# Kernel tuning notes

Measured on AMD Instinct MI355X. Metric: run time of the kernel, lower is better.

## Reference

```python
import jax, jax.numpy as jnp
import numpy as np

SEQ_LEN = 2048
D_MODEL = 1024
K = 32
B = 16
CP = K * (K + 1) // 2  # 528


def _spectral_filters(seq_len: int, k: int) -> np.ndarray:
    # Hankel matrix Z_ij = 2 / ((i+j)^3 - (i+j)), 1-indexed
    e = np.arange(1, seq_len + 1, dtype=np.float64)
    ipj = e[:, None] + e[None, :]
    Z = 2.0 / (ipj ** 3 - ipj)
    sigma, phi = np.linalg.eigh(Z)
    sk = np.clip(sigma[-k:], 1e-9, None)
    return (phi[:, -k:] * sk ** 0.25).astype(np.float32)


# static upper-triangular index pattern and sqrt(2) off-diagonal scaling
_IU0, _IU1 = np.triu_indices(K)
_SCALE = np.where(_IU0 == _IU1, 1.0, np.sqrt(2.0)).astype(np.float32)


def setup_inputs() -> dict:
    key = jax.random.key(0)
    ks = jax.random.split(key, 8)
    filters = jnp.asarray(_spectral_filters(SEQ_LEN, K))
    x = jax.random.normal(ks[0], (B, SEQ_LEN, D_MODEL), dtype=jnp.float32)
    pre_w = jax.random.normal(ks[1], (SEQ_LEN, D_MODEL), dtype=jnp.float32) / np.sqrt(D_MODEL)
    pre_b = jnp.zeros((SEQ_LEN,), dtype=jnp.float32)
    qp_w = jax.random.normal(ks[2], (CP, K), dtype=jnp.float32) / np.sqrt(K)
    qp_b = jnp.zeros((CP,), dtype=jnp.float32)
    o_w = jax.random.normal(ks[3], (D_MODEL, CP), dtype=jnp.float32) / np.sqrt(CP)
    o_b = jnp.zeros((D_MODEL,), dtype=jnp.float32)
    decay = jnp.ones((SEQ_LEN,), dtype=jnp.float32)
    return {
        'x': x,
        'pre_w': pre_w, 'pre_b': pre_b,
        'q_filters': filters,          # learnable copy
        'k_filters': filters,          # fixed buffer copy
        'qp_w': qp_w, 'qp_b': qp_b,
        'o_w': o_w, 'o_b': o_b,
        'decay': decay,
    }


def reference(x, pre_w, pre_b, q_filters, k_filters, qp_w, qp_b, o_w, o_b, decay):
    # pre_proj: (B,T,d_model) -> (B,T,seq_len)
    x_proj = x @ pre_w.T + pre_b
    # spectral projections onto top-K filters: (B,T,K)
    Q = jnp.einsum('bti,ik->btk', x_proj, q_filters)
    Q = Q @ qp_w.T + qp_b                      # (B,T,CP)
    V = jnp.einsum('bti,ik->btk', x_proj, k_filters)
    # symmetric outer product compressed to upper triangle, off-diag * sqrt(2)
    iu0 = jnp.asarray(_IU0)
    iu1 = jnp.asarray(_IU1)
    scale = jnp.asarray(_SCALE)
    Z = V[..., iu0] * V[..., iu1] * scale      # (B,T,CP), avoids (B,T,K,K)
    Z = Z * decay[None, :, None]
    H = jnp.cumsum(Z, axis=1)                  # causal state accumulation
    Y = Q * H
    return Y @ o_w.T + o_b                     # (B,T,d_model)
```

## Files before the change

### kernel.cpp

```cpp
#include <hip/hip_runtime.h>
#include <hip/hip_bf16.h>
#include <math.h>

#define T_SEQ   2048
#define DM      1024
#define KF      32
#define BATCH   16
#define CPDIM   528
#define KPAD    544
#define YSTR    552
#define QVSTR   36
#define MROWS   (BATCH * T_SEQ)
#define NCHUNK  32
#define TCHUNK  64

typedef __bf16 bf16x8 __attribute__((ext_vector_type(8)));
typedef float f32x4 __attribute__((ext_vector_type(4)));
typedef unsigned uint2v __attribute__((ext_vector_type(2)));

__device__ __forceinline__ unsigned packsplit(float v) {
  unsigned u = __float_as_uint(v);
  unsigned h = (u + 0x7fffu + ((u >> 16) & 1u)) & 0xffff0000u;
  float rr = v - __uint_as_float(h);
  return h | (__float_as_uint(rr) >> 16);
}

__device__ __forceinline__ unsigned short f2bf(float f) {
  unsigned u = __float_as_uint(f);
  return (unsigned short)((u + 0x7fffu + ((u >> 16) & 1u)) >> 16);
}
__device__ __forceinline__ float bf2f(unsigned short h) {
  return __uint_as_float((unsigned)h << 16);
}

__device__ __forceinline__ void gload16(const void* g, void* l) {
  __builtin_amdgcn_global_load_lds(
      (const __attribute__((address_space(1))) unsigned*)g,
      (__attribute__((address_space(3))) unsigned*)l, 16, 0, 0);
}

__global__ __launch_bounds__(256) void k_fold_part(const float* __restrict__ pre_w,
                                                   const float* __restrict__ qf,
                                                   const float* __restrict__ kfil,
                                                   float* __restrict__ Wp) {
  const int sc = blockIdx.x;
  const int it = blockIdx.y;
  const int s0 = sc * 64, i0 = it * 64;
  const int tid = threadIdx.x;
  __shared__ float fs[64][64];
  __shared__ float ps[64][64];
  for (int idx = tid; idx < 4096; idx += 256) {
    const int s = idx >> 6, c = idx & 63;
    fs[s][c] = (c < KF) ? qf[(s0 + s) * KF + c] : kfil[(s0 + s) * KF + c - KF];
    ps[s][c] = pre_w[(size_t)(s0 + s) * DM + i0 + c];
  }
  __syncthreads();
  const int i = tid & 63;
  const int kb = tid >> 6;
  float acc[16] = {};
  for (int s = 0; s < 64; ++s) {
    const float pv = ps[s][i];
    const float4 f0 = *reinterpret_cast<const float4*>(&fs[s][kb * 16 + 0]);
    const float4 f1 = *reinterpret_cast<const float4*>(&fs[s][kb * 16 + 4]);
    const float4 f2 = *reinterpret_cast<const float4*>(&fs[s][kb * 16 + 8]);
    const float4 f3 = *reinterpret_cast<const float4*>(&fs[s][kb * 16 + 12]);
    acc[0]  = fmaf(pv, f0.x, acc[0]);  acc[1]  = fmaf(pv, f0.y, acc[1]);
    acc[2]  = fmaf(pv, f0.z, acc[2]);  acc[3]  = fmaf(pv, f0.w, acc[3]);
    acc[4]  = fmaf(pv, f1.x, acc[4]);  acc[5]  = fmaf(pv, f1.y, acc[5]);
    acc[6]  = fmaf(pv, f1.z, acc[6]);  acc[7]  = fmaf(pv, f1.w, acc[7]);
    acc[8]  = fmaf(pv, f2.x, acc[8]);  acc[9]  = fmaf(pv, f2.y, acc[9]);
    acc[10] = fmaf(pv, f2.z, acc[10]); acc[11] = fmaf(pv, f2.w, acc[11]);
    acc[12] = fmaf(pv, f3.x, acc[12]); acc[13] = fmaf(pv, f3.y, acc[13]);
    acc[14] = fmaf(pv, f3.z, acc[14]); acc[15] = fmaf(pv, f3.w, acc[15]);
  }
#pragma unroll
  for (int j = 0; j < 16; ++j)
    Wp[((size_t)sc * 64 + kb * 16 + j) * DM + i0 + i] = acc[j];
}

__global__ __launch_bounds__(256) void k_foldred_bias(const float* __restrict__ Wp,
                                                      const float* __restrict__ pre_b,
                                                      const float* __restrict__ qf,
                                                      const float* __restrict__ kfil,
                                                      unsigned short* __restrict__ Wt_hi,
                                                      unsigned short* __restrict__ Wt_lo,
                                                      float* __restrict__ bias64) {
  if (blockIdx.x == 256) {
    __shared__ float part[4][64];
    const int k = threadIdx.x & 63;
    const int q = threadIdx.x >> 6;
    float acc = 0.f;
    for (int s = q * 512; s < (q + 1) * 512; ++s) {
      const float fv = (k < KF) ? qf[s * KF + k] : kfil[s * KF + k - KF];
      acc = fmaf(pre_b[s], fv, acc);
    }
    part[q][k] = acc;
    __syncthreads();
    if (threadIdx.x < 64)
      bias64[threadIdx.x] = part[0][k] + part[1][k] + part[2][k] + part[3][k];
    return;
  }
  const int idx = blockIdx.x * 256 + threadIdx.x;
  float acc = 0.f;
#pragma unroll
  for (int sc = 0; sc < NCHUNK; ++sc)
    acc += Wp[(size_t)sc * 64 * DM + idx];
  const unsigned pk = packsplit(acc);
  Wt_hi[idx] = (unsigned short)(pk >> 16);
  Wt_lo[idx] = (unsigned short)(pk & 0xffffu);
}

__global__ __launch_bounds__(256) void k_q0v_cs(const float* __restrict__ x,
                                                const unsigned short* __restrict__ Wt_hi,
                                                const unsigned short* __restrict__ Wt_lo,
                                                const float* __restrict__ bias64,
                                                const float* __restrict__ decay,
                                                float* __restrict__ Q0V,
                                                float* __restrict__ S) {
  __shared__ float Xs[3][64 * 32];
  __shared__ unsigned short Wh[3][64 * 32];
  __shared__ unsigned short Wl[3][64 * 32];
  __shared__ float vs2[64 * 32];
  __shared__ float dec2[64];
  const int tid = threadIdx.x;
  const int m0 = blockIdx.x * 64;
  const int w = tid >> 6, l = tid & 63;
  const int g = l >> 4, r = l & 15;

  f32x4 acc[4] = {};

  auto stage = [&](int buf, int k0) {
#pragma unroll
    for (int q = 0; q < 2; ++q) {
      const int c = q * 256 + tid;
      const int row = c >> 3, sl = c & 7;
      const int col4 = (sl ^ (row & 7)) * 4;
      gload16(&x[(size_t)(m0 + row) * DM + k0 + col4], &Xs[buf][c * 4]);
    }
    {
      const int row = tid >> 2, sl = tid & 3;
      const int colh = (sl ^ ((row >> 1) & 3)) * 8;
      gload16(&Wt_hi[(size_t)row * DM + k0 + colh], &Wh[buf][tid * 8]);
      gload16(&Wt_lo[(size_t)row * DM + k0 + colh], &Wl[buf][tid * 8]);
    }
  };

  auto compute = [&](int cur) {
    const int arow = w * 16 + r;
    const int sx = (2 * g) ^ (arow & 7);
    const int sy = (2 * g + 1) ^ (arow & 7);
    const f32x4 pX = *reinterpret_cast<const f32x4*>(&Xs[cur][arow * 32 + sx * 4]);
    const f32x4 pY = *reinterpret_cast<const f32x4*>(&Xs[cur][arow * 32 + sy * 4]);
    unsigned pk[8];
#pragma unroll
    for (int e = 0; e < 4; ++e) { pk[e] = packsplit(pX[e]); pk[4 + e] = packsplit(pY[e]); }
    union { unsigned u[4]; bf16x8 v; } ah, al;
#pragma unroll
    for (int j = 0; j < 4; ++j) {
      ah.u[j] = (pk[2 * j] >> 16) | (pk[2 * j + 1] & 0xffff0000u);
      al.u[j] = (pk[2 * j] & 0xffffu) | (pk[2 * j + 1] << 16);
    }
    bf16x8 bh[4], bl[4];
#pragma unroll
    for (int n = 0; n < 4; ++n) {
      const int brow = n * 16 + r;
      const int bs = g ^ ((brow >> 1) & 3);
      const int off = brow * 32 + bs * 8;
      bh[n] = *reinterpret_cast<const bf16x8*>(&Wh[cur][off]);
      bl[n] = *reinterpret_cast<const bf16x8*>(&Wl[cur][off]);
    }
#pragma unroll
    for (int n = 0; n < 4; ++n) {
      acc[n] = __builtin_amdgcn_mfma_f32_16x16x32_bf16(bh[n], ah.v, acc[n], 0, 0, 0);
      acc[n] = __builtin_amdgcn_mfma_f32_16x16x32_bf16(bh[n], al.v, acc[n], 0, 0, 0);
      acc[n] = __builtin_amdgcn_mfma_f32_16x16x32_bf16(bl[n], ah.v, acc[n], 0, 0, 0);
    }
  };

  if (tid < 64) dec2[tid] = decay[(m0 & 2047) + tid];

  stage(0, 0);
  stage(1, 32);

  for (int base = 0; base < 30; base += 3) {
#pragma unroll
    for (int sub = 0; sub < 3; ++sub) {
      const int it = base + sub;
      asm volatile("s_waitcnt vmcnt(4)" ::: "memory");
      __builtin_amdgcn_s_barrier();
      __builtin_amdgcn_sched_barrier(0);
      stage((sub + 2) % 3, (it + 2) * 32);
      compute(sub);
    }
  }
  asm volatile("s_waitcnt vmcnt(4)" ::: "memory");
  __builtin_amdgcn_s_barrier();
  __builtin_amdgcn_sched_barrier(0);
  compute(0);
  asm volatile("s_waitcnt vmcnt(0)" ::: "memory");
  __builtin_amdgcn_s_barrier();
  __builtin_amdgcn_sched_barrier(0);
  compute(1);

  const int trow = w * 16 + r;
  const int row_o = m0 + trow;
#pragma unroll
  for (int n = 0; n < 4; ++n) {
    const int col_o = n * 16 + g * 4;
    const float4 bb = *reinterpret_cast<const float4*>(&bias64[col_o]);
    float4 v;
    v.x = acc[n][0] + bb.x; v.y = acc[n][1] + bb.y;
    v.z = acc[n][2] + bb.z; v.w = acc[n][3] + bb.w;
    *reinterpret_cast<float4*>(&Q0V[(size_t)row_o * 64 + col_o]) = v;
    if (n >= 2)
      *reinterpret_cast<float4*>(&vs2[trow * 32 + (n - 2) * 16 + g * 4]) = v;
  }
  __syncthreads();

  const int b = m0 >> 11, ch = (m0 & 2047) >> 6;
#pragma unroll
  for (int pass = 0; pass < 3; ++pass) {
    const int c = tid + pass * 256;
    if (c < CPDIM) {
      int i = 0, rem = c;
      while (rem >= KF - i) { rem -= KF - i; ++i; }
      const int j = i + rem;
      const float sc = (i == j) ? 1.0f : 1.41421356237309515f;
      float h = 0.f;
#pragma unroll 4
      for (int t = 0; t < TCHUNK; ++t)
        h = fmaf(vs2[t * KF + i] * vs2[t * KF + j], dec2[t], h);
      S[(size_t)(b * NCHUNK + ch) * CPDIM + c] = h * sc;
    }
  }
}

__global__ __launch_bounds__(576) void k_scanchunks(float* __restrict__ S) {
  const int b = blockIdx.x;
  const int c = threadIdx.x;
  if (c >= CPDIM) return;
  float v[NCHUNK];
#pragma unroll
  for (int ch = 0; ch < NCHUNK; ++ch)
    v[ch] = S[(size_t)(b * NCHUNK + ch) * CPDIM + c];
  float run = 0.f;
#pragma unroll
  for (int ch = 0; ch < NCHUNK; ++ch) {
    S[(size_t)(b * NCHUNK + ch) * CPDIM + c] = run;
    run += v[ch];
  }
}

#define NB_OWB  (DM * KPAD / 256)
#define NB_QPW  (KPAD * KF / 256)
__global__ __launch_bounds__(256) void k_prep(const float* __restrict__ ow,
                                              const float* __restrict__ qp_w,
                                              const float* __restrict__ qp_b,
                                              unsigned short* __restrict__ owb,
                                              unsigned short* __restrict__ qpw_hi,
                                              unsigned short* __restrict__ qpw_lo,
                                              float* __restrict__ qpb_pad) {
  const int bx = blockIdx.x;
  if (bx < NB_OWB) {
    const int idx = bx * 256 + threadIdx.x;
    const int n = idx / KPAD, k = idx - n * KPAD;
    owb[idx] = (k < CPDIM) ? f2bf(ow[(size_t)n * CPDIM + k]) : (unsigned short)0;
  } else if (bx < NB_OWB + NB_QPW) {
    const int idx = (bx - NB_OWB) * 256 + threadIdx.x;
    const int c = idx >> 5;
    unsigned pk = 0;
    if (c < CPDIM) pk = packsplit(qp_w[idx]);
    qpw_hi[idx] = (unsigned short)(pk >> 16);
    qpw_lo[idx] = (unsigned short)(pk & 0xffffu);
  } else {
    for (int c = threadIdx.x; c < KPAD; c += 256)
      qpb_pad[c] = (c < CPDIM) ? qp_b[c] : 0.f;
  }
}

__global__ __launch_bounds__(1024, 4) void k_out_fused(const float* __restrict__ Q0V,
                                                       const float* __restrict__ S,
                                                       const unsigned short* __restrict__ qpw_hi,
                                                       const unsigned short* __restrict__ qpw_lo,
                                                       const float* __restrict__ qpb_pad,
                                                       const float* __restrict__ decay,
                                                       const unsigned short* __restrict__ owb,
                                                       const float* __restrict__ ob,
                                                       float* __restrict__ out) {
  __shared__ float vs[64 * QVSTR];
  __shared__ float dec[64];
  __shared__ unsigned short Ylds[64 * YSTR];
  const int tid = threadIdx.x;
  const int m0 = blockIdx.x * 64;
  const int b = m0 >> 11, ch = (m0 & 2047) >> 6;
  const int t0 = m0 & 2047;
  const int wv = tid >> 6, l = tid & 63;
  const int g = l >> 4, r = l & 15;

  if (tid < 512) {
    const int row = tid >> 3, c4 = tid & 7;
    const float4 v = *reinterpret_cast<const float4*>(&Q0V[(size_t)(m0 + row) * 64 + 32 + c4 * 4]);
    *reinterpret_cast<float4*>(&vs[row * QVSTR + c4 * 4]) = v;
  }
  if (tid < 64) dec[tid] = decay[t0 + tid];

  {
    bf16x8 qah[4], qal[4];
#pragma unroll
    for (int m = 0; m < 4; ++m) {
      const int t = m * 16 + r;
      const f32x4 x0 = *reinterpret_cast<const f32x4*>(&Q0V[(size_t)(m0 + t) * 64 + g * 8]);
      const f32x4 x1 = *reinterpret_cast<const f32x4*>(&Q0V[(size_t)(m0 + t) * 64 + g * 8 + 4]);
      unsigned pk[8];
#pragma unroll
      for (int e = 0; e < 4; ++e) { pk[e] = packsplit(x0[e]); pk[4 + e] = packsplit(x1[e]); }
      union { unsigned u[4]; bf16x8 v; } hh, ll;
#pragma unroll
      for (int j = 0; j < 4; ++j) {
        hh.u[j] = (pk[2 * j] >> 16) | (pk[2 * j + 1] & 0xffff0000u);
        ll.u[j] = (pk[2 * j] & 0xffffu) | (pk[2 * j + 1] << 16);
      }
      qah[m] = hh.v; qal[m] = ll.v;
    }
    for (int nt = wv; nt < KPAD / 16; nt += 16) {
      const int crow = nt * 16 + r;
      const bf16x8 bh = *reinterpret_cast<const bf16x8*>(&qpw_hi[crow * KF + g * 8]);
      const bf16x8 bl = *reinterpret_cast<const bf16x8*>(&qpw_lo[crow * KF + g * 8]);
      const int cbase = nt * 16 + g * 4;
      const float4 qb4 = *reinterpret_cast<const float4*>(&qpb_pad[cbase]);
      f32x4 a[4];
#pragma unroll
      for (int m = 0; m < 4; ++m) { a[m][0] = qb4.x; a[m][1] = qb4.y; a[m][2] = qb4.z; a[m][3] = qb4.w; }
#pragma unroll
      for (int m = 0; m < 4; ++m) {
        a[m] = __builtin_amdgcn_mfma_f32_16x16x32_bf16(bh, qah[m], a[m], 0, 0, 0);
        a[m] = __builtin_amdgcn_mfma_f32_16x16x32_bf16(bh, qal[m], a[m], 0, 0, 0);
        a[m] = __builtin_amdgcn_mfma_f32_16x16x32_bf16(bl, qah[m], a[m], 0, 0, 0);
      }
#pragma unroll
      for (int m = 0; m < 4; ++m) {
        const int t = m * 16 + r;
        union { unsigned short s[4]; unsigned u[2]; } pk4;
#pragma unroll
        for (int j = 0; j < 4; ++j) pk4.s[j] = f2bf(a[m][j]);
        *reinterpret_cast<uint2v*>(&Ylds[t * YSTR + cbase]) = uint2v{pk4.u[0], pk4.u[1]};
      }
    }
  }
  __syncthreads();

  if (tid < CPDIM) {
    const int c = tid;
    int i = 0, rem = c;
    while (rem >= KF - i) { rem -= KF - i; ++i; }
    const int j = i + rem;
    const float sc = (i == j) ? 1.0f : 1.41421356237309515f;
    float h = S[(size_t)(b * NCHUNK + ch) * CPDIM + c];
    for (int t = 0; t < TCHUNK; ++t) {
      h = fmaf(vs[t * QVSTR + i] * vs[t * QVSTR + j] * sc, dec[t], h);
      const float qv = bf2f(Ylds[t * YSTR + c]);
      Ylds[t * YSTR + c] = f2bf(qv * h);
    }
  }
  __syncthreads();

  f32x4 acc[4][4] = {};
  for (int ks = 0; ks <= 16; ++ks) {
    const int kh = ks * 32 + g * 8;
    bf16x8 bf4[4], af[4];
#pragma unroll
    for (int n = 0; n < 4; ++n)
      bf4[n] = *reinterpret_cast<const bf16x8*>(&owb[(size_t)(wv * 64 + n * 16 + r) * KPAD + kh]);
#pragma unroll
    for (int m = 0; m < 4; ++m)
      af[m] = *reinterpret_cast<const bf16x8*>(&Ylds[(m * 16 + r) * YSTR + kh]);
#pragma unroll
    for (int m = 0; m < 4; ++m)
#pragma unroll
      for (int n = 0; n < 4; ++n)
        acc[m][n] = __builtin_amdgcn_mfma_f32_16x16x32_bf16(bf4[n], af[m], acc[m][n], 0, 0, 0);
  }

#pragma unroll
  for (int m = 0; m < 4; ++m) {
    const int row_o = m0 + m * 16 + r;
#pragma unroll
    for (int n = 0; n < 4; ++n) {
      const int col_o = wv * 64 + n * 16 + g * 4;
      const float4 bb = *reinterpret_cast<const float4*>(&ob[col_o]);
      float4 v;
      v.x = acc[m][n][0] + bb.x; v.y = acc[m][n][1] + bb.y;
      v.z = acc[m][n][2] + bb.z; v.w = acc[m][n][3] + bb.w;
      *reinterpret_cast<float4*>(&out[(size_t)row_o * DM + col_o]) = v;
    }
  }
}

extern "C" void kernel_launch(void* const* d_in, const int* in_sizes, int n_in,
                              void* d_out, int out_size, void* d_ws, size_t ws_size,
                              hipStream_t stream) {
  const float* x      = (const float*)d_in[0];
  const float* pre_w  = (const float*)d_in[1];
  const float* pre_b  = (const float*)d_in[2];
  const float* q_filt = (const float*)d_in[3];
  const float* k_filt = (const float*)d_in[4];
  const float* qp_w   = (const float*)d_in[5];
  const float* qp_b   = (const float*)d_in[6];
  const float* o_w    = (const float*)d_in[7];
  const float* o_b    = (const float*)d_in[8];
  const float* decay  = (const float*)d_in[9];
  float* out = (float*)d_out;

  char* ws = (char*)d_ws;
  unsigned short* Wt_hi = (unsigned short*)(ws);
  unsigned short* Wt_lo = (unsigned short*)(ws + 131072);
  float*    bias64 = (float*)(ws + 262144);
  float*    Q0V    = (float*)(ws + 262400);
  float*    S      = (float*)(ws + 8651008);
  unsigned short* owb = (unsigned short*)(ws + 9732352);
  unsigned short* qpw_hi = (unsigned short*)(ws + 10846464);
  unsigned short* qpw_lo = (unsigned short*)(ws + 10881280);
  float*    qpb_pad = (float*)(ws + 10916096);
  float*    Wp     = (float*)(ws + 16777216);

  k_fold_part<<<dim3(NCHUNK, 16), dim3(256), 0, stream>>>(pre_w, q_filt, k_filt, Wp);
  k_foldred_bias<<<dim3(257), dim3(256), 0, stream>>>(Wp, pre_b, q_filt, k_filt, Wt_hi, Wt_lo, bias64);
  k_q0v_cs<<<dim3(MROWS / 64), dim3(256), 0, stream>>>(x, Wt_hi, Wt_lo, bias64, decay, Q0V, S);
  k_scanchunks<<<dim3(BATCH), dim3(576), 0, stream>>>(S);
  k_prep<<<dim3(NB_OWB + NB_QPW + 1), dim3(256), 0, stream>>>(o_w, qp_w, qp_b, owb, qpw_hi, qpw_lo, qpb_pad);
  k_out_fused<<<dim3(MROWS / 64), dim3(1024), 0, stream>>>(Q0V, S, qpw_hi, qpw_lo, qpb_pad, decay, owb, o_b, out);
}
```

Before: 184.6 us.

## Double k_q0v_cs threads and read V/decay directly from global in out kernel

```diff
diff --git a/kernel.cpp b/kernel.cpp
--- a/kernel.cpp
+++ b/kernel.cpp
@@ -9,7 +9,6 @@
 #define CPDIM   528
 #define KPAD    544
 #define YSTR    552
-#define QVSTR   36
 #define MROWS   (BATCH * T_SEQ)
 #define NCHUNK  32
 #define TCHUNK  64
@@ -110,7 +109,7 @@
   Wt_lo[idx] = (unsigned short)(pk & 0xffffu);
 }
 
-__global__ __launch_bounds__(256) void k_q0v_cs(const float* __restrict__ x,
+__global__ __launch_bounds__(512) void k_q0v_cs(const float* __restrict__ x,
                                                 const unsigned short* __restrict__ Wt_hi,
                                                 const unsigned short* __restrict__ Wt_lo,
                                                 const float* __restrict__ bias64,
@@ -126,27 +125,29 @@
   const int m0 = blockIdx.x * 64;
   const int w = tid >> 6, l = tid & 63;
   const int g = l >> 4, r = l & 15;
-
-  f32x4 acc[4] = {};
+  const int wr = w & 3, wh = w >> 2;
+
+  f32x4 acc[2] = {};
 
   auto stage = [&](int buf, int k0) {
-#pragma unroll
-    for (int q = 0; q < 2; ++q) {
-      const int c = q * 256 + tid;
-      const int row = c >> 3, sl = c & 7;
+    {
+      const int row = tid >> 3, sl = tid & 7;
       const int col4 = (sl ^ (row & 7)) * 4;
-      gload16(&x[(size_t)(m0 + row) * DM + k0 + col4], &Xs[buf][c * 4]);
+      gload16(&x[(size_t)(m0 + row) * DM + k0 + col4], &Xs[buf][tid * 4]);
     }
     {
-      const int row = tid >> 2, sl = tid & 3;
+      const int c2 = tid & 255;
+      const int row = c2 >> 2, sl = c2 & 3;
       const int colh = (sl ^ ((row >> 1) & 3)) * 8;
-      gload16(&Wt_hi[(size_t)row * DM + k0 + colh], &Wh[buf][tid * 8]);
-      gload16(&Wt_lo[(size_t)row * DM + k0 + colh], &Wl[buf][tid * 8]);
+      unsigned short* dst = (tid < 256) ? &Wh[buf][c2 * 8] : &Wl[buf][c2 * 8];
+      const unsigned short* src = (tid < 256) ? &Wt_hi[(size_t)row * DM + k0 + colh]
+                                              : &Wt_lo[(size_t)row * DM + k0 + colh];
+      gload16(src, dst);
     }
   };
 
   auto compute = [&](int cur) {
-    const int arow = w * 16 + r;
+    const int arow = wr * 16 + r;
     const int sx = (2 * g) ^ (arow & 7);
     const int sy = (2 * g + 1) ^ (arow & 7);
     const f32x4 pX = *reinterpret_cast<const f32x4*>(&Xs[cur][arow * 32 + sx * 4]);
@@ -160,20 +161,20 @@
       ah.u[j] = (pk[2 * j] >> 16) | (pk[2 * j + 1] & 0xffff0000u);
       al.u[j] = (pk[2 * j] & 0xffffu) | (pk[2 * j + 1] << 16);
     }
-    bf16x8 bh[4], bl[4];
-#pragma unroll
-    for (int n = 0; n < 4; ++n) {
-      const int brow = n * 16 + r;
+    bf16x8 bh[2], bl[2];
+#pragma unroll
+    for (int nb = 0; nb < 2; ++nb) {
+      const int brow = (wh * 2 + nb) * 16 + r;
       const int bs = g ^ ((brow >> 1) & 3);
       const int off = brow * 32 + bs * 8;
-      bh[n] = *reinterpret_cast<const bf16x8*>(&Wh[cur][off]);
-      bl[n] = *reinterpret_cast<const bf16x8*>(&Wl[cur][off]);
-    }
-#pragma unroll
-    for (int n = 0; n < 4; ++n) {
-      acc[n] = __builtin_amdgcn_mfma_f32_16x16x32_bf16(bh[n], ah.v, acc[n], 0, 0, 0);
-      acc[n] = __builtin_amdgcn_mfma_f32_16x16x32_bf16(bh[n], al.v, acc[n], 0, 0, 0);
-      acc[n] = __builtin_amdgcn_mfma_f32_16x16x32_bf16(bl[n], ah.v, acc[n], 0, 0, 0);
+      bh[nb] = *reinterpret_cast<const bf16x8*>(&Wh[cur][off]);
+      bl[nb] = *reinterpret_cast<const bf16x8*>(&Wl[cur][off]);
+    }
+#pragma unroll
+    for (int nb = 0; nb < 2; ++nb) {
+      acc[nb] = __builtin_amdgcn_mfma_f32_16x16x32_bf16(bh[nb], ah.v, acc[nb], 0, 0, 0);
+      acc[nb] = __builtin_amdgcn_mfma_f32_16x16x32_bf16(bh[nb], al.v, acc[nb], 0, 0, 0);
+      acc[nb] = __builtin_amdgcn_mfma_f32_16x16x32_bf16(bl[nb], ah.v, acc[nb], 0, 0, 0);
     }
   };
 
@@ -186,14 +187,14 @@
 #pragma unroll
     for (int sub = 0; sub < 3; ++sub) {
       const int it = base + sub;
-      asm volatile("s_waitcnt vmcnt(4)" ::: "memory");
+      asm volatile("s_waitcnt vmcnt(2)" ::: "memory");
       __builtin_amdgcn_s_barrier();
       __builtin_amdgcn_sched_barrier(0);
       stage((sub + 2) % 3, (it + 2) * 32);
       compute(sub);
     }
   }
-  asm volatile("s_waitcnt vmcnt(4)" ::: "memory");
+  asm volatile("s_waitcnt vmcnt(2)" ::: "memory");
   __builtin_amdgcn_s_barrier();
   __builtin_amdgcn_sched_barrier(0);
   compute(0);
@@ -202,15 +203,16 @@
   __builtin_amdgcn_sched_barrier(0);
   compute(1);
 
-  const int trow = w * 16 + r;
+  const int trow = wr * 16 + r;
   const int row_o = m0 + trow;
 #pragma unroll
-  for (int n = 0; n < 4; ++n) {
+  for (int nb = 0; nb < 2; ++nb) {
+    const int n = wh * 2 + nb;
     const int col_o = n * 16 + g * 4;
     const float4 bb = *reinterpret_cast<const float4*>(&bias64[col_o]);
     float4 v;
-    v.x = acc[n][0] + bb.x; v.y = acc[n][1] + bb.y;
-    v.z = acc[n][2] + bb.z; v.w = acc[n][3] + bb.w;
+    v.x = acc[nb][0] + bb.x; v.y = acc[nb][1] + bb.y;
+    v.z = acc[nb][2] + bb.z; v.w = acc[nb][3] + bb.w;
     *reinterpret_cast<float4*>(&Q0V[(size_t)row_o * 64 + col_o]) = v;
     if (n >= 2)
       *reinterpret_cast<float4*>(&vs2[trow * 32 + (n - 2) * 16 + g * 4]) = v;
@@ -219,8 +221,8 @@
 
   const int b = m0 >> 11, ch = (m0 & 2047) >> 6;
 #pragma unroll
-  for (int pass = 0; pass < 3; ++pass) {
-    const int c = tid + pass * 256;
+  for (int pass = 0; pass < 2; ++pass) {
+    const int c = tid + pass * 512;
     if (c < CPDIM) {
       int i = 0, rem = c;
       while (rem >= KF - i) { rem -= KF - i; ++i; }
@@ -287,8 +289,6 @@
                                                        const unsigned short* __restrict__ owb,
                                                        const float* __restrict__ ob,
                                                        float* __restrict__ out) {
-  __shared__ float vs[64 * QVSTR];
-  __shared__ float dec[64];
   __shared__ unsigned short Ylds[64 * YSTR];
   const int tid = threadIdx.x;
   const int m0 = blockIdx.x * 64;
@@ -297,13 +297,6 @@
   const int wv = tid >> 6, l = tid & 63;
   const int g = l >> 4, r = l & 15;
 
-  if (tid < 512) {
-    const int row = tid >> 3, c4 = tid & 7;
-    const float4 v = *reinterpret_cast<const float4*>(&Q0V[(size_t)(m0 + row) * 64 + 32 + c4 * 4]);
-    *reinterpret_cast<float4*>(&vs[row * QVSTR + c4 * 4]) = v;
-  }
-  if (tid < 64) dec[tid] = decay[t0 + tid];
-
   {
     bf16x8 qah[4], qal[4];
 #pragma unroll
@@ -355,9 +348,13 @@
     while (rem >= KF - i) { rem -= KF - i; ++i; }
     const int j = i + rem;
     const float sc = (i == j) ? 1.0f : 1.41421356237309515f;
+    const float* vrow = &Q0V[(size_t)m0 * 64 + 32];
     float h = S[(size_t)(b * NCHUNK + ch) * CPDIM + c];
+#pragma unroll 8
     for (int t = 0; t < TCHUNK; ++t) {
-      h = fmaf(vs[t * QVSTR + i] * vs[t * QVSTR + j] * sc, dec[t], h);
+      const float vi = vrow[t * 64 + i];
+      const float vj = vrow[t * 64 + j];
+      h = fmaf(vi * vj * sc, decay[t0 + t], h);
       const float qv = bf2f(Ylds[t * YSTR + c]);
       Ylds[t * YSTR + c] = f2bf(qv * h);
     }
@@ -425,7 +422,7 @@
 
   k_fold_part<<<dim3(NCHUNK, 16), dim3(256), 0, stream>>>(pre_w, q_filt, k_filt, Wp);
   k_foldred_bias<<<dim3(257), dim3(256), 0, stream>>>(Wp, pre_b, q_filt, k_filt, Wt_hi, Wt_lo, bias64);
-  k_q0v_cs<<<dim3(MROWS / 64), dim3(256), 0, stream>>>(x, Wt_hi, Wt_lo, bias64, decay, Q0V, S);
+  k_q0v_cs<<<dim3(MROWS / 64), dim3(512), 0, stream>>>(x, Wt_hi, Wt_lo, bias64, decay, Q0V, S);
   k_scanchunks<<<dim3(BATCH), dim3(576), 0, stream>>>(S);
   k_prep<<<dim3(NB_OWB + NB_QPW + 1), dim3(256), 0, stream>>>(o_w, qp_w, qp_b, owb, qpw_hi, qpw_lo, qpb_pad);
   k_out_fused<<<dim3(MROWS / 64), dim3(1024), 0, stream>>>(Q0V, S, qpw_hi, qpw_lo, qpb_pad, decay, owb, o_b, out);
```

Measured after the change: 176.5 us. 1.05x faster.
